# Optimization experiments

Hardware: AMD Instinct MI355X
Metric: run time of the kernel (lower is better)

Reference implementation:

```python
import jax, jax.numpy as jnp
import numpy as np

EPS = 1e-6

def _l2norm(t):
    # F.normalize over channel axis (axis=1) of (B, dk, L)
    n = jnp.sqrt(jnp.sum(t * t, axis=1, keepdims=True))
    return t / jnp.maximum(n, EPS)

def setup_inputs() -> dict:
    key = jax.random.key(0)
    ks = jax.random.split(key, 8)
    B, Cin, Cenc, dk, dv, H, W = 2, 64, 96, 64, 64, 96, 96
    return {
        "x": jax.random.normal(ks[0], (B, Cin, H, W), dtype=jnp.float32),
        "x_enc": jax.random.normal(ks[1], (B, Cenc, H, W), dtype=jnp.float32),
        "Wq": jax.random.normal(ks[2], (dk, Cenc), dtype=jnp.float32) * 0.05,
        "bq": jax.random.normal(ks[3], (dk,), dtype=jnp.float32) * 0.05,
        "Wk": jax.random.normal(ks[4], (dk, Cenc), dtype=jnp.float32) * 0.05,
        "bk": jax.random.normal(ks[5], (dk,), dtype=jnp.float32) * 0.05,
        "Wv": jax.random.normal(ks[6], (dv, Cin), dtype=jnp.float32) * 0.05,
        "bv": jax.random.normal(ks[7], (dv,), dtype=jnp.float32) * 0.05,
    }

def reference(x, x_enc, Wq, bq, Wk, bk, Wv, bv):
    B, _, H, W = x.shape
    L = H * W
    # 1x1 conv projections == channel matmuls, then flatten spatial dims
    Q = (jnp.einsum('bchw,kc->bkhw', x_enc, Wq) + bq[None, :, None, None]).reshape(B, -1, L)
    K = (jnp.einsum('bchw,kc->bkhw', x_enc, Wk) + bk[None, :, None, None]).reshape(B, -1, L)
    V = (jnp.einsum('bchw,kc->bkhw', x, Wv) + bv[None, :, None, None]).reshape(B, -1, L)
    # per-position L2 normalization over the dk channel axis ('l2' mode)
    Q = _l2norm(Q)
    K = _l2norm(K)
    # A[b,i,j] = sum_q Q[b,q,i] * K[b,q,j], softmax over j
    A = jax.nn.softmax(jnp.einsum('bqi,bqj->bij', Q, K), axis=-1)  # (B, L, L)
    R = jnp.einsum('bij,bvj->bvi', A, V)  # (B, dv, L)
    return R.reshape(B, -1, H, W)
```

## Files before the change

### kernel.cpp

```cpp
#include <hip/hip_runtime.h>
#include <hip/hip_bf16.h>
#include <math.h>

#define NB   2
#define CIN  64
#define CENC 96
#define DK   64
#define DV   64
#define LL   9216
#define QBLK 128
#define KVBLK 64
#define NQT  (LL/QBLK)
#define LOG2E 1.44269504088896340736f

typedef __attribute__((ext_vector_type(8))) short short8;
typedef __attribute__((ext_vector_type(4))) float f32x4;
typedef __attribute__((ext_vector_type(2))) unsigned int uint2v;
typedef unsigned int uint;

__device__ inline void gload16(const void* g, void* l) {
    __builtin_amdgcn_global_load_lds(
        (const __attribute__((address_space(1))) unsigned int*)g,
        (__attribute__((address_space(3))) unsigned int*)l, 16, 0, 0);
}

__device__ inline unsigned short f2bf(float f) {
    union { float f; uint u; } v; v.f = f;
    uint r = (v.u + 0x7FFFu + ((v.u >> 16) & 1u)) >> 16;
    return (unsigned short)r;
}

__device__ inline uint pack_bf16x2(float lo, float hi) {
    __hip_bfloat162 h = __float22bfloat162_rn(float2{lo, hi});
    union { __hip_bfloat162 h; uint u; } cvt; cvt.h = h;
    return cvt.u;
}

__global__ __launch_bounds__(256) void proj_qk_kernel(
    const float* __restrict__ x_enc,
    const float* __restrict__ Wq, const float* __restrict__ bq,
    const float* __restrict__ Wk, const float* __restrict__ bk,
    unsigned short* __restrict__ Qb, unsigned short* __restrict__ Kb)
{
    __shared__ float Wt[2][CENC * 64];
    const int tid = threadIdx.x;
    for (int idx = tid; idx < DK * CENC; idx += 256) {
        int k = idx / CENC, c = idx - k * CENC;
        Wt[0][c * 64 + (k ^ (c & 31))] = Wq[idx];
        Wt[1][c * 64 + (k ^ (c & 31))] = Wk[idx];
    }
    __syncthreads();

    const int w    = __builtin_amdgcn_readfirstlane(tid >> 6);
    const int lane = tid & 63;
    const int gw   = blockIdx.x * 4 + w;
    const int p0g  = gw * 16;
    const int b    = p0g / LL;
    const int p0   = p0g - b * LL;

    float qa[16], ka[16];
    const float bqv = bq[lane], bkv = bk[lane];
#pragma unroll
    for (int p = 0; p < 16; ++p) { qa[p] = bqv; ka[p] = bkv; }

    const float* xp = x_enc + (size_t)b * CENC * LL + p0;
#pragma unroll 4
    for (int c = 0; c < CENC; ++c) {
        const float wq = Wt[0][c * 64 + (lane ^ (c & 31))];
        const float wk = Wt[1][c * 64 + (lane ^ (c & 31))];
        const float* xc = xp + (size_t)c * LL;
#pragma unroll
        for (int p = 0; p < 16; ++p) {
            const float xv = xc[p];
            qa[p] = fmaf(wq, xv, qa[p]);
            ka[p] = fmaf(wk, xv, ka[p]);
        }
    }

    unsigned short* qrow = Qb + (size_t)(b * LL + p0) * 64 + lane;
    unsigned short* krow = Kb + (size_t)(b * LL + p0) * 64 + lane;
#pragma unroll
    for (int p = 0; p < 16; ++p) {
        float sq = qa[p] * qa[p];
        float sk = ka[p] * ka[p];
#pragma unroll
        for (int m = 1; m < 64; m <<= 1) {
            sq += __shfl_xor(sq, m, 64);
            sk += __shfl_xor(sk, m, 64);
        }
        qrow[(size_t)p * 64] = f2bf(qa[p] * (1.f / fmaxf(sqrtf(sq), 1e-6f)));
        krow[(size_t)p * 64] = f2bf(ka[p] * (1.f / fmaxf(sqrtf(sk), 1e-6f)));
    }
}

__global__ __launch_bounds__(256) void proj_v_kernel(
    const float* __restrict__ x,
    const float* __restrict__ Wv, const float* __restrict__ bv,
    unsigned short* __restrict__ Vt)
{
    __shared__ float Wt[CIN * 64];
    __shared__ unsigned short Vl[64 * 64];
    const int tid = threadIdx.x;
    for (int idx = tid; idx < DV * CIN; idx += 256) {
        int v = idx / CIN, c = idx - v * CIN;
        Wt[c * 64 + (v ^ (c & 31))] = Wv[idx];
    }
    __syncthreads();

    const int w    = __builtin_amdgcn_readfirstlane(tid >> 6);
    const int lane = tid & 63;
    const int l0g  = blockIdx.x * 64;
    const int b    = l0g / LL;
    const int l0   = l0g - b * LL;
    const int p0   = w * 16;

    float va[16];
    const float bvv = bv[lane];
#pragma unroll
    for (int p = 0; p < 16; ++p) va[p] = bvv;

    const float* xp = x + (size_t)b * CIN * LL + l0 + p0;
#pragma unroll 4
    for (int c = 0; c < CIN; ++c) {
        const float wv = Wt[c * 64 + (lane ^ (c & 31))];
        const float* xc = xp + (size_t)c * LL;
#pragma unroll
        for (int p = 0; p < 16; ++p) va[p] = fmaf(wv, xc[p], va[p]);
    }
#pragma unroll
    for (int p = 0; p < 16; ++p) Vl[(p0 + p) * 64 + lane] = f2bf(va[p]);
    __syncthreads();

    const int v = tid & 63, w2 = tid >> 6;
    uint pk[8];
#pragma unroll
    for (int j = 0; j < 8; ++j)
        pk[j] = (uint)Vl[(w2 * 16 + 2 * j) * 64 + v] |
                ((uint)Vl[(w2 * 16 + 2 * j + 1) * 64 + v] << 16);
    uint4* dst = (uint4*)(Vt + (size_t)b * 64 * LL + (size_t)v * LL + l0 + w2 * 16);
    dst[0] = make_uint4(pk[0], pk[1], pk[2], pk[3]);
    dst[1] = make_uint4(pk[4], pk[5], pk[6], pk[7]);
}

__global__ __launch_bounds__(256, 3) void flash_kernel(
    const unsigned short* __restrict__ Qb,
    const unsigned short* __restrict__ Kb,
    const unsigned short* __restrict__ Vt,
    float* __restrict__ Sp, float* __restrict__ Rp,
    int JS, int nt)
{
    __shared__ unsigned short Kl[2][KVBLK * 64];
    __shared__ unsigned short Vl[2][64 * KVBLK];
    __shared__ unsigned short Pl[4 * 32 * 64];

    const int bid0  = blockIdx.x;
    const int chunk = gridDim.x >> 3;
    const int bid   = (bid0 & 7) * chunk + (bid0 >> 3);

    const int qt  = bid % NQT;
    const int js  = (bid / NQT) % JS;
    const int b   = bid / (NQT * JS);
    const int tid = threadIdx.x;
    const int w = tid >> 6, lane = tid & 63;
    const int li = lane & 15, hi = lane >> 4;
    const int i0 = qt * QBLK + w * 32;

    short8 qf[2][2];
#pragma unroll
    for (int it = 0; it < 2; ++it)
#pragma unroll
        for (int kc = 0; kc < 2; ++kc)
            qf[it][kc] = *(const short8*)(Qb + ((size_t)(b * LL + i0 + it * 16 + li)) * 64 + hi * 8 + kc * 32);

    const int a0 = li * 128 + (( hi     ) ^ (li & 7)) * 16;
    const int a1 = li * 128 + ((hi + 4) ^ (li & 7)) * 16;

    const int o0 = w * 1024 + lane * 16;
    const int o1 = o0 + 4096;
    const int r0 = o0 >> 7, r1 = o1 >> 7;
    const int c0 = ((o0 >> 4) & 7) ^ (r0 & 7);
    const int c1 = ((o1 >> 4) & 7) ^ (r1 & 7);

    const unsigned short* KbB = Kb + (size_t)b * LL * 64;
    const unsigned short* VtB = Vt + (size_t)b * 64 * LL;

    f32x4 racc[2][4];
#pragma unroll
    for (int it = 0; it < 2; ++it)
#pragma unroll
        for (int vt = 0; vt < 4; ++vt)
            racc[it][vt] = (f32x4){0.f, 0.f, 0.f, 0.f};
    float ssum[2] = {0.f, 0.f};

    char* Plw = (char*)Pl + w * 4096;

    int j0 = js * (nt * KVBLK);
    gload16(KbB + (size_t)(j0 + r0) * 64 + c0 * 8, (char*)Kl[0] + w * 1024);
    gload16(KbB + (size_t)(j0 + r1) * 64 + c1 * 8, (char*)Kl[0] + w * 1024 + 4096);
    gload16(VtB + (size_t)r0 * LL + j0 + c0 * 8, (char*)Vl[0] + w * 1024);
    gload16(VtB + (size_t)r1 * LL + j0 + c1 * 8, (char*)Vl[0] + w * 1024 + 4096);

    for (int t = 0; t < nt; ++t, j0 += KVBLK) {
        __syncthreads();
        const int bb = t & 1;
        if (t + 1 < nt) {
            const int j1 = j0 + KVBLK;
            gload16(KbB + (size_t)(j1 + r0) * 64 + c0 * 8, (char*)Kl[bb ^ 1] + w * 1024);
            gload16(KbB + (size_t)(j1 + r1) * 64 + c1 * 8, (char*)Kl[bb ^ 1] + w * 1024 + 4096);
            gload16(VtB + (size_t)r0 * LL + j1 + c0 * 8, (char*)Vl[bb ^ 1] + w * 1024);
            gload16(VtB + (size_t)r1 * LL + j1 + c1 * 8, (char*)Vl[bb ^ 1] + w * 1024 + 4096);
        }
        const char* Klb = (const char*)Kl[bb];
        const char* Vlb = (const char*)Vl[bb];

#pragma unroll
        for (int jt = 0; jt < 4; ++jt) {
            const short8 k0 = *(const short8*)(Klb + jt * 2048 + a0);
            const short8 k1 = *(const short8*)(Klb + jt * 2048 + a1);
#pragma unroll
            for (int it = 0; it < 2; ++it) {
                f32x4 acc = (f32x4){0.f, 0.f, 0.f, 0.f};
                acc = __builtin_amdgcn_mfma_f32_16x16x32_bf16(k0, qf[it][0], acc, 0, 0, 0);
                acc = __builtin_amdgcn_mfma_f32_16x16x32_bf16(k1, qf[it][1], acc, 0, 0, 0);
                float p0 = __builtin_amdgcn_exp2f(fmaf(acc[0], LOG2E, -LOG2E));
                float p1 = __builtin_amdgcn_exp2f(fmaf(acc[1], LOG2E, -LOG2E));
                float p2 = __builtin_amdgcn_exp2f(fmaf(acc[2], LOG2E, -LOG2E));
                float p3 = __builtin_amdgcn_exp2f(fmaf(acc[3], LOG2E, -LOG2E));
                ssum[it] += (p0 + p1) + (p2 + p3);
                uint2v u;
                u.x = pack_bf16x2(p0, p1);
                u.y = pack_bf16x2(p2, p3);
                *(uint2v*)(Plw + (it * 16 + li) * 128
                               + (((jt * 2 + (hi >> 1)) ^ (li & 7)) * 16) + (hi & 1) * 8) = u;
            }
        }
        __asm__ volatile("" ::: "memory");

#pragma unroll
        for (int jc = 0; jc < 2; ++jc) {
            const short8 pa0 = *(const short8*)(Plw + (0 * 16 + li) * 128 + (((jc * 4 + hi) ^ (li & 7)) * 16));
            const short8 pa1 = *(const short8*)(Plw + (1 * 16 + li) * 128 + (((jc * 4 + hi) ^ (li & 7)) * 16));
            const int av = jc ? a1 : a0;
#pragma unroll
            for (int vt = 0; vt < 4; ++vt) {
                const short8 vb = *(const short8*)(Vlb + vt * 2048 + av);
                racc[0][vt] = __builtin_amdgcn_mfma_f32_16x16x32_bf16(pa0, vb, racc[0][vt], 0, 0, 0);
                racc[1][vt] = __builtin_amdgcn_mfma_f32_16x16x32_bf16(pa1, vb, racc[1][vt], 0, 0, 0);
            }
        }
        __asm__ volatile("" ::: "memory");
    }

#pragma unroll
    for (int it = 0; it < 2; ++it) {
        float s = ssum[it];
        s += __shfl_xor(s, 16, 64);
        s += __shfl_xor(s, 32, 64);
        if (hi == 0) Sp[(size_t)(b * JS + js) * LL + i0 + it * 16 + li] = s;
    }
    const size_t rBase = (size_t)(b * JS + js) * 64;
#pragma unroll
    for (int it = 0; it < 2; ++it)
#pragma unroll
        for (int vt = 0; vt < 4; ++vt) {
            float4 val = make_float4(racc[it][vt][0], racc[it][vt][1], racc[it][vt][2], racc[it][vt][3]);
            *(float4*)&Rp[(rBase + vt * 16 + li) * LL + i0 + it * 16 + hi * 4] = val;
        }
}

__global__ __launch_bounds__(256) void combine_kernel(
    const float* __restrict__ Sp, const float* __restrict__ Rp,
    float* __restrict__ out, int JS)
{
    size_t g4 = ((size_t)blockIdx.x * 256 + threadIdx.x) * 4;
    int l = (int)(g4 % LL);
    int v = (int)((g4 / LL) % 64);
    int b = (int)(g4 / ((size_t)64 * LL));
    float4 s = make_float4(0.f, 0.f, 0.f, 0.f);
    float4 r = make_float4(0.f, 0.f, 0.f, 0.f);
    for (int js = 0; js < JS; ++js) {
        const float4 sv = *(const float4*)&Sp[(size_t)(b * JS + js) * LL + l];
        const float4 rv = *(const float4*)&Rp[((size_t)(b * JS + js) * 64 + v) * LL + l];
        s.x += sv.x; s.y += sv.y; s.z += sv.z; s.w += sv.w;
        r.x += rv.x; r.y += rv.y; r.z += rv.z; r.w += rv.w;
    }
    *(float4*)&out[g4] = make_float4(r.x / s.x, r.y / s.y, r.z / s.z, r.w / s.w);
}

extern "C" void kernel_launch(void* const* d_in, const int* in_sizes, int n_in,
                              void* d_out, int out_size, void* d_ws, size_t ws_size,
                              hipStream_t stream) {
    (void)in_sizes; (void)n_in; (void)out_size;
    const float* x     = (const float*)d_in[0];
    const float* x_enc = (const float*)d_in[1];
    const float* Wq    = (const float*)d_in[2];
    const float* bq    = (const float*)d_in[3];
    const float* Wk    = (const float*)d_in[4];
    const float* bk    = (const float*)d_in[5];
    const float* Wv    = (const float*)d_in[6];
    const float* bv    = (const float*)d_in[7];
    float* out = (float*)d_out;
    char* ws = (char*)d_ws;

    const size_t nBF = (size_t)NB * LL * 64 * 2;
    unsigned short* Qb = (unsigned short*)ws;
    unsigned short* Kb = (unsigned short*)(ws + nBF);
    unsigned short* Vt = (unsigned short*)(ws + 2 * nBF);

    int JS = 8;
    while (JS > 1) {
        size_t need = 3 * nBF + (size_t)NB * JS * LL * 4 + (size_t)NB * JS * 64 * LL * 4;
        if (need <= ws_size) break;
        JS >>= 1;
    }
    float* Sp = (float*)(ws + 3 * nBF);
    float* Rp = Sp + (size_t)NB * JS * LL;
    int nt = (LL / JS) / KVBLK;

    proj_qk_kernel<<<NB * LL / 64, 256, 0, stream>>>(x_enc, Wq, bq, Wk, bk, Qb, Kb);
    proj_v_kernel <<<NB * LL / 64, 256, 0, stream>>>(x, Wv, bv, Vt);
    flash_kernel  <<<NB * JS * NQT, 256, 0, stream>>>(Qb, Kb, Vt, Sp, Rp, JS, nt);
    combine_kernel<<<(NB * 64 * LL) / 1024, 256, 0, stream>>>(Sp, Rp, out, JS);
}
```

Before: 117.6 us.

## Switch flash kernel to 32x32 MFMA with register-resident P and fused projection

The attention kernel moves from 16x16x32 to 32x32x16 bf16 MFMA tiles with 64 queries per wave and a 256-query block. The softmax probabilities are repacked in registers with permlane32 swaps instead of going through a shared-memory P buffer. LOG2E is folded into the Q normalization so the exp2 needs no extra FMA, and s_setprio is set around the MFMA groups. The Q/K and V projections are merged into one launch, and the key split rises to 12. The cost is higher register pressure, occupancy capped at 2 blocks per CU, and a larger partial-result buffer for the combine step.

```diff
diff --git a/kernel.cpp b/kernel.cpp
--- a/kernel.cpp
+++ b/kernel.cpp
@@ -8,14 +8,14 @@
 #define DK   64
 #define DV   64
 #define LL   9216
-#define QBLK 128
+#define QBLK 256
 #define KVBLK 64
 #define NQT  (LL/QBLK)
 #define LOG2E 1.44269504088896340736f
 
-typedef __attribute__((ext_vector_type(8))) short short8;
-typedef __attribute__((ext_vector_type(4))) float f32x4;
-typedef __attribute__((ext_vector_type(2))) unsigned int uint2v;
+typedef __attribute__((ext_vector_type(8)))  short short8;
+typedef __attribute__((ext_vector_type(16))) float f32x16;
+typedef __attribute__((ext_vector_type(2)))  unsigned int uint2v;
 typedef unsigned int uint;
 
 __device__ inline void gload16(const void* g, void* l) {
@@ -36,113 +36,127 @@
     return cvt.u;
 }
 
-__global__ __launch_bounds__(256) void proj_qk_kernel(
-    const float* __restrict__ x_enc,
+__device__ inline void plswap(uint& a, uint& b) {
+#if __has_builtin(__builtin_amdgcn_permlane32_swap)
+    uint2v r = __builtin_amdgcn_permlane32_swap(a, b, false, false);
+    a = r.x; b = r.y;
+#else
+    const int lane = threadIdx.x & 63;
+    uint t = (lane < 32) ? b : a;
+    t = __shfl_xor(t, 32, 64);
+    uint an = (lane < 32) ? a : t;
+    uint bn = (lane < 32) ? t : b;
+    a = an; b = bn;
+#endif
+}
+
+__global__ __launch_bounds__(256) void proj_kernel(
+    const float* __restrict__ x, const float* __restrict__ x_enc,
     const float* __restrict__ Wq, const float* __restrict__ bq,
     const float* __restrict__ Wk, const float* __restrict__ bk,
-    unsigned short* __restrict__ Qb, unsigned short* __restrict__ Kb)
+    const float* __restrict__ Wv, const float* __restrict__ bv,
+    unsigned short* __restrict__ Qb, unsigned short* __restrict__ Kb,
+    unsigned short* __restrict__ Vt, int nqk)
 {
-    __shared__ float Wt[2][CENC * 64];
+    __shared__ float sh[2 * CENC * 64];
     const int tid = threadIdx.x;
-    for (int idx = tid; idx < DK * CENC; idx += 256) {
-        int k = idx / CENC, c = idx - k * CENC;
-        Wt[0][c * 64 + (k ^ (c & 31))] = Wq[idx];
-        Wt[1][c * 64 + (k ^ (c & 31))] = Wk[idx];
-    }
-    __syncthreads();
-
-    const int w    = __builtin_amdgcn_readfirstlane(tid >> 6);
-    const int lane = tid & 63;
-    const int gw   = blockIdx.x * 4 + w;
-    const int p0g  = gw * 16;
-    const int b    = p0g / LL;
-    const int p0   = p0g - b * LL;
-
-    float qa[16], ka[16];
-    const float bqv = bq[lane], bkv = bk[lane];
-#pragma unroll
-    for (int p = 0; p < 16; ++p) { qa[p] = bqv; ka[p] = bkv; }
-
-    const float* xp = x_enc + (size_t)b * CENC * LL + p0;
+
+    if ((int)blockIdx.x < nqk) {
+        float* Wt0 = sh;
+        float* Wt1 = sh + CENC * 64;
+        for (int idx = tid; idx < DK * CENC; idx += 256) {
+            int k = idx / CENC, c = idx - k * CENC;
+            Wt0[c * 64 + (k ^ (c & 31))] = Wq[idx];
+            Wt1[c * 64 + (k ^ (c & 31))] = Wk[idx];
+        }
+        __syncthreads();
+
+        const int w    = __builtin_amdgcn_readfirstlane(tid >> 6);
+        const int lane = tid & 63;
+        const int gw   = blockIdx.x * 4 + w;
+        const int p0g  = gw * 16;
+        const int b    = p0g / LL;
+        const int p0   = p0g - b * LL;
+
+        float qa[16], ka[16];
+        const float bqv = bq[lane], bkv = bk[lane];
+#pragma unroll
+        for (int p = 0; p < 16; ++p) { qa[p] = bqv; ka[p] = bkv; }
+
+        const float* xp = x_enc + (size_t)b * CENC * LL + p0;
 #pragma unroll 4
-    for (int c = 0; c < CENC; ++c) {
-        const float wq = Wt[0][c * 64 + (lane ^ (c & 31))];
-        const float wk = Wt[1][c * 64 + (lane ^ (c & 31))];
-        const float* xc = xp + (size_t)c * LL;
+        for (int c = 0; c < CENC; ++c) {
+            const float wq = Wt0[c * 64 + (lane ^ (c & 31))];
+            const float wk = Wt1[c * 64 + (lane ^ (c & 31))];
+            const float* xc = xp + (size_t)c * LL;
+#pragma unroll
+            for (int p = 0; p < 16; ++p) {
+                const float xv = xc[p];
+                qa[p] = fmaf(wq, xv, qa[p]);
+                ka[p] = fmaf(wk, xv, ka[p]);
+            }
+        }
+
+        unsigned short* qrow = Qb + (size_t)(b * LL + p0) * 64 + lane;
+        unsigned short* krow = Kb + (size_t)(b * LL + p0) * 64 + lane;
 #pragma unroll
         for (int p = 0; p < 16; ++p) {
-            const float xv = xc[p];
-            qa[p] = fmaf(wq, xv, qa[p]);
-            ka[p] = fmaf(wk, xv, ka[p]);
-        }
-    }
-
-    unsigned short* qrow = Qb + (size_t)(b * LL + p0) * 64 + lane;
-    unsigned short* krow = Kb + (size_t)(b * LL + p0) * 64 + lane;
-#pragma unroll
-    for (int p = 0; p < 16; ++p) {
-        float sq = qa[p] * qa[p];
-        float sk = ka[p] * ka[p];
-#pragma unroll
-        for (int m = 1; m < 64; m <<= 1) {
-            sq += __shfl_xor(sq, m, 64);
-            sk += __shfl_xor(sk, m, 64);
-        }
-        qrow[(size_t)p * 64] = f2bf(qa[p] * (1.f / fmaxf(sqrtf(sq), 1e-6f)));
-        krow[(size_t)p * 64] = f2bf(ka[p] * (1.f / fmaxf(sqrtf(sk), 1e-6f)));
-    }
-}
-
-__global__ __launch_bounds__(256) void proj_v_kernel(
-    const float* __restrict__ x,
-    const float* __restrict__ Wv, const float* __restrict__ bv,
-    unsigned short* __restrict__ Vt)
-{
-    __shared__ float Wt[CIN * 64];
-    __shared__ unsigned short Vl[64 * 64];
-    const int tid = threadIdx.x;
-    for (int idx = tid; idx < DV * CIN; idx += 256) {
-        int v = idx / CIN, c = idx - v * CIN;
-        Wt[c * 64 + (v ^ (c & 31))] = Wv[idx];
-    }
-    __syncthreads();
-
-    const int w    = __builtin_amdgcn_readfirstlane(tid >> 6);
-    const int lane = tid & 63;
-    const int l0g  = blockIdx.x * 64;
-    const int b    = l0g / LL;
-    const int l0   = l0g - b * LL;
-    const int p0   = w * 16;
-
-    float va[16];
-    const float bvv = bv[lane];
-#pragma unroll
-    for (int p = 0; p < 16; ++p) va[p] = bvv;
-
-    const float* xp = x + (size_t)b * CIN * LL + l0 + p0;
+            float sq = qa[p] * qa[p];
+            float sk = ka[p] * ka[p];
+#pragma unroll
+            for (int m = 1; m < 64; m <<= 1) {
+                sq += __shfl_xor(sq, m, 64);
+                sk += __shfl_xor(sk, m, 64);
+            }
+            qrow[(size_t)p * 64] = f2bf(qa[p] * (LOG2E / fmaxf(sqrtf(sq), 1e-6f)));
+            krow[(size_t)p * 64] = f2bf(ka[p] * (1.f / fmaxf(sqrtf(sk), 1e-6f)));
+        }
+    } else {
+        float* Wt = sh;
+        unsigned short* Vsh = (unsigned short*)(sh + CIN * 64);
+        for (int idx = tid; idx < DV * CIN; idx += 256) {
+            int v = idx / CIN, c = idx - v * CIN;
+            Wt[c * 64 + (v ^ (c & 31))] = Wv[idx];
+        }
+        __syncthreads();
+
+        const int w    = __builtin_amdgcn_readfirstlane(tid >> 6);
+        const int lane = tid & 63;
+        const int l0g  = ((int)blockIdx.x - nqk) * 64;
+        const int b    = l0g / LL;
+        const int l0   = l0g - b * LL;
+        const int p0   = w * 16;
+
+        float va[16];
+        const float bvv = bv[lane];
+#pragma unroll
+        for (int p = 0; p < 16; ++p) va[p] = bvv;
+
+        const float* xp = x + (size_t)b * CIN * LL + l0 + p0;
 #pragma unroll 4
-    for (int c = 0; c < CIN; ++c) {
-        const float wv = Wt[c * 64 + (lane ^ (c & 31))];
-        const float* xc = xp + (size_t)c * LL;
-#pragma unroll
-        for (int p = 0; p < 16; ++p) va[p] = fmaf(wv, xc[p], va[p]);
-    }
-#pragma unroll
-    for (int p = 0; p < 16; ++p) Vl[(p0 + p) * 64 + lane] = f2bf(va[p]);
-    __syncthreads();
-
-    const int v = tid & 63, w2 = tid >> 6;
-    uint pk[8];
-#pragma unroll
-    for (int j = 0; j < 8; ++j)
-        pk[j] = (uint)Vl[(w2 * 16 + 2 * j) * 64 + v] |
-                ((uint)Vl[(w2 * 16 + 2 * j + 1) * 64 + v] << 16);
-    uint4* dst = (uint4*)(Vt + (size_t)b * 64 * LL + (size_t)v * LL + l0 + w2 * 16);
-    dst[0] = make_uint4(pk[0], pk[1], pk[2], pk[3]);
-    dst[1] = make_uint4(pk[4], pk[5], pk[6], pk[7]);
-}
-
-__global__ __launch_bounds__(256, 3) void flash_kernel(
+        for (int c = 0; c < CIN; ++c) {
+            const float wv = Wt[c * 64 + (lane ^ (c & 31))];
+            const float* xc = xp + (size_t)c * LL;
+#pragma unroll
+            for (int p = 0; p < 16; ++p) va[p] = fmaf(wv, xc[p], va[p]);
+        }
+#pragma unroll
+        for (int p = 0; p < 16; ++p) Vsh[(p0 + p) * 64 + lane] = f2bf(va[p]);
+        __syncthreads();
+
+        const int v = tid & 63, w2 = tid >> 6;
+        uint pk[8];
+#pragma unroll
+        for (int j = 0; j < 8; ++j)
+            pk[j] = (uint)Vsh[(w2 * 16 + 2 * j) * 64 + v] |
+                    ((uint)Vsh[(w2 * 16 + 2 * j + 1) * 64 + v] << 16);
+        uint4* dst = (uint4*)(Vt + (size_t)b * 64 * LL + (size_t)v * LL + l0 + w2 * 16);
+        dst[0] = make_uint4(pk[0], pk[1], pk[2], pk[3]);
+        dst[1] = make_uint4(pk[4], pk[5], pk[6], pk[7]);
+    }
+}
+
+__global__ __launch_bounds__(256, 2) void flash_kernel(
     const unsigned short* __restrict__ Qb,
     const unsigned short* __restrict__ Kb,
     const unsigned short* __restrict__ Vt,
@@ -151,7 +165,6 @@
 {
     __shared__ unsigned short Kl[2][KVBLK * 64];
     __shared__ unsigned short Vl[2][64 * KVBLK];
-    __shared__ unsigned short Pl[4 * 32 * 64];
 
     const int bid0  = blockIdx.x;
     const int chunk = gridDim.x >> 3;
@@ -162,18 +175,15 @@
     const int b   = bid / (NQT * JS);
     const int tid = threadIdx.x;
     const int w = tid >> 6, lane = tid & 63;
-    const int li = lane & 15, hi = lane >> 4;
-    const int i0 = qt * QBLK + w * 32;
-
-    short8 qf[2][2];
-#pragma unroll
-    for (int it = 0; it < 2; ++it)
-#pragma unroll
-        for (int kc = 0; kc < 2; ++kc)
-            qf[it][kc] = *(const short8*)(Qb + ((size_t)(b * LL + i0 + it * 16 + li)) * 64 + hi * 8 + kc * 32);
-
-    const int a0 = li * 128 + (( hi     ) ^ (li & 7)) * 16;
-    const int a1 = li * 128 + ((hi + 4) ^ (li & 7)) * 16;
+    const int ln = lane & 31, h = lane >> 5;
+    const int i0w = qt * QBLK + w * 64;
+
+    short8 qf[2][4];
+#pragma unroll
+    for (int ig = 0; ig < 2; ++ig)
+#pragma unroll
+        for (int kc = 0; kc < 4; ++kc)
+            qf[ig][kc] = *(const short8*)(Qb + ((size_t)(b * LL + i0w + ig * 32 + ln)) * 64 + kc * 16 + h * 8);
 
     const int o0 = w * 1024 + lane * 16;
     const int o1 = o0 + 4096;
@@ -184,17 +194,16 @@
     const unsigned short* KbB = Kb + (size_t)b * LL * 64;
     const unsigned short* VtB = Vt + (size_t)b * 64 * LL;
 
-    f32x4 racc[2][4];
-#pragma unroll
-    for (int it = 0; it < 2; ++it)
-#pragma unroll
-        for (int vt = 0; vt < 4; ++vt)
-            racc[it][vt] = (f32x4){0.f, 0.f, 0.f, 0.f};
+    f32x16 racc[2][2];
+#pragma unroll
+    for (int ig = 0; ig < 2; ++ig)
+#pragma unroll
+        for (int vg = 0; vg < 2; ++vg)
+#pragma unroll
+            for (int r = 0; r < 16; ++r) racc[ig][vg][r] = 0.f;
     float ssum[2] = {0.f, 0.f};
 
-    char* Plw = (char*)Pl + w * 4096;
-
-    int j0 = js * (nt * KVBLK);
+    int j0 = js * nt * KVBLK;
     gload16(KbB + (size_t)(j0 + r0) * 64 + c0 * 8, (char*)Kl[0] + w * 1024);
     gload16(KbB + (size_t)(j0 + r1) * 64 + c1 * 8, (char*)Kl[0] + w * 1024 + 4096);
     gload16(VtB + (size_t)r0 * LL + j0 + c0 * 8, (char*)Vl[0] + w * 1024);
@@ -214,57 +223,84 @@
         const char* Vlb = (const char*)Vl[bb];
 
 #pragma unroll
-        for (int jt = 0; jt < 4; ++jt) {
-            const short8 k0 = *(const short8*)(Klb + jt * 2048 + a0);
-            const short8 k1 = *(const short8*)(Klb + jt * 2048 + a1);
-#pragma unroll
-            for (int it = 0; it < 2; ++it) {
-                f32x4 acc = (f32x4){0.f, 0.f, 0.f, 0.f};
-                acc = __builtin_amdgcn_mfma_f32_16x16x32_bf16(k0, qf[it][0], acc, 0, 0, 0);
-                acc = __builtin_amdgcn_mfma_f32_16x16x32_bf16(k1, qf[it][1], acc, 0, 0, 0);
-                float p0 = __builtin_amdgcn_exp2f(fmaf(acc[0], LOG2E, -LOG2E));
-                float p1 = __builtin_amdgcn_exp2f(fmaf(acc[1], LOG2E, -LOG2E));
-                float p2 = __builtin_amdgcn_exp2f(fmaf(acc[2], LOG2E, -LOG2E));
-                float p3 = __builtin_amdgcn_exp2f(fmaf(acc[3], LOG2E, -LOG2E));
-                ssum[it] += (p0 + p1) + (p2 + p3);
-                uint2v u;
-                u.x = pack_bf16x2(p0, p1);
-                u.y = pack_bf16x2(p2, p3);
-                *(uint2v*)(Plw + (it * 16 + li) * 128
-                               + (((jt * 2 + (hi >> 1)) ^ (li & 7)) * 16) + (hi & 1) * 8) = u;
-            }
-        }
-        __asm__ volatile("" ::: "memory");
-
-#pragma unroll
-        for (int jc = 0; jc < 2; ++jc) {
-            const short8 pa0 = *(const short8*)(Plw + (0 * 16 + li) * 128 + (((jc * 4 + hi) ^ (li & 7)) * 16));
-            const short8 pa1 = *(const short8*)(Plw + (1 * 16 + li) * 128 + (((jc * 4 + hi) ^ (li & 7)) * 16));
-            const int av = jc ? a1 : a0;
-#pragma unroll
-            for (int vt = 0; vt < 4; ++vt) {
-                const short8 vb = *(const short8*)(Vlb + vt * 2048 + av);
-                racc[0][vt] = __builtin_amdgcn_mfma_f32_16x16x32_bf16(pa0, vb, racc[0][vt], 0, 0, 0);
-                racc[1][vt] = __builtin_amdgcn_mfma_f32_16x16x32_bf16(pa1, vb, racc[1][vt], 0, 0, 0);
-            }
-        }
-        __asm__ volatile("" ::: "memory");
-    }
-
-#pragma unroll
-    for (int it = 0; it < 2; ++it) {
-        float s = ssum[it];
-        s += __shfl_xor(s, 16, 64);
-        s += __shfl_xor(s, 32, 64);
-        if (hi == 0) Sp[(size_t)(b * JS + js) * LL + i0 + it * 16 + li] = s;
+        for (int jt = 0; jt < 2; ++jt) {
+            f32x16 sacc[2];
+#pragma unroll
+            for (int ig = 0; ig < 2; ++ig)
+#pragma unroll
+                for (int r = 0; r < 16; ++r) sacc[ig][r] = 0.f;
+
+            __builtin_amdgcn_s_setprio(1);
+#pragma unroll
+            for (int kc = 0; kc < 4; ++kc) {
+                const int rowK = jt * 32 + ln;
+                const short8 kf = *(const short8*)(Klb + rowK * 128 + (((kc << 1) + h) ^ (rowK & 7)) * 16);
+                sacc[0] = __builtin_amdgcn_mfma_f32_32x32x16_bf16(kf, qf[0][kc], sacc[0], 0, 0, 0);
+                sacc[1] = __builtin_amdgcn_mfma_f32_32x32x16_bf16(kf, qf[1][kc], sacc[1], 0, 0, 0);
+            }
+            __builtin_amdgcn_s_setprio(0);
+
+            short8 pf[2][2];
+#pragma unroll
+            for (int ig = 0; ig < 2; ++ig) {
+                float p[16];
+#pragma unroll
+                for (int r = 0; r < 16; ++r) p[r] = __builtin_amdgcn_exp2f(sacc[ig][r]);
+                float s0 = 0.f;
+#pragma unroll
+                for (int r = 0; r < 16; r += 4) s0 += (p[r] + p[r + 1]) + (p[r + 2] + p[r + 3]);
+                ssum[ig] += s0;
+                uint u0[4], u1[4];
+#pragma unroll
+                for (int g = 0; g < 4; ++g) {
+                    u0[g] = pack_bf16x2(p[4 * g], p[4 * g + 1]);
+                    u1[g] = pack_bf16x2(p[4 * g + 2], p[4 * g + 3]);
+                }
+#pragma unroll
+                for (int c = 0; c < 2; ++c) {
+                    uint a0 = u0[2 * c], b0 = u0[2 * c + 1];
+                    uint a1 = u1[2 * c], b1 = u1[2 * c + 1];
+                    plswap(a0, b0);
+                    plswap(a1, b1);
+                    union { uint u[4]; short8 s; } P;
+                    P.u[0] = a0; P.u[1] = a1; P.u[2] = b0; P.u[3] = b1;
+                    pf[ig][c] = P.s;
+                }
+            }
+
+            __builtin_amdgcn_s_setprio(1);
+#pragma unroll
+            for (int c = 0; c < 2; ++c) {
+                const int kcv = 2 * jt + c;
+#pragma unroll
+                for (int vg = 0; vg < 2; ++vg) {
+                    const int rowV = vg * 32 + ln;
+                    const short8 vf = *(const short8*)(Vlb + rowV * 128 + (((kcv << 1) + h) ^ (rowV & 7)) * 16);
+                    racc[0][vg] = __builtin_amdgcn_mfma_f32_32x32x16_bf16(pf[0][c], vf, racc[0][vg], 0, 0, 0);
+                    racc[1][vg] = __builtin_amdgcn_mfma_f32_32x32x16_bf16(pf[1][c], vf, racc[1][vg], 0, 0, 0);
+                }
+            }
+            __builtin_amdgcn_s_setprio(0);
+        }
+    }
+
+#pragma unroll
+    for (int ig = 0; ig < 2; ++ig) {
+        float s = ssum[ig] + __shfl_xor(ssum[ig], 32, 64);
+        if (h == 0) Sp[(size_t)(b * JS + js) * LL + i0w + ig * 32 + ln] = s;
     }
     const size_t rBase = (size_t)(b * JS + js) * 64;
 #pragma unroll
-    for (int it = 0; it < 2; ++it)
-#pragma unroll
-        for (int vt = 0; vt < 4; ++vt) {
-            float4 val = make_float4(racc[it][vt][0], racc[it][vt][1], racc[it][vt][2], racc[it][vt][3]);
-            *(float4*)&Rp[(rBase + vt * 16 + li) * LL + i0 + it * 16 + hi * 4] = val;
+    for (int ig = 0; ig < 2; ++ig)
+#pragma unroll
+        for (int vg = 0; vg < 2; ++vg) {
+            float* dst = Rp + (rBase + vg * 32 + ln) * (size_t)LL + i0w + ig * 32 + 4 * h;
+#pragma unroll
+            for (int rr = 0; rr < 4; ++rr) {
+                float4 val = make_float4(racc[ig][vg][4 * rr + 0], racc[ig][vg][4 * rr + 1],
+                                         racc[ig][vg][4 * rr + 2], racc[ig][vg][4 * rr + 3]);
+                *(float4*)&dst[8 * rr] = val;
+            }
         }
 }
 
@@ -307,18 +343,21 @@
     unsigned short* Kb = (unsigned short*)(ws + nBF);
     unsigned short* Vt = (unsigned short*)(ws + 2 * nBF);
 
-    int JS = 8;
-    while (JS > 1) {
-        size_t need = 3 * nBF + (size_t)NB * JS * LL * 4 + (size_t)NB * JS * 64 * LL * 4;
-        if (need <= ws_size) break;
-        JS >>= 1;
+    int JS = 12;
+    {
+        const int cand[3] = {12, 8, 4};
+        for (int ci = 0; ci < 3; ++ci) {
+            JS = cand[ci];
+            size_t need = 3 * nBF + (size_t)NB * JS * LL * 4 + (size_t)NB * JS * 64 * LL * 4;
+            if (need <= ws_size) break;
+        }
     }
     float* Sp = (float*)(ws + 3 * nBF);
     float* Rp = Sp + (size_t)NB * JS * LL;
     int nt = (LL / JS) / KVBLK;
 
-    proj_qk_kernel<<<NB * LL / 64, 256, 0, stream>>>(x_enc, Wq, bq, Wk, bk, Qb, Kb);
-    proj_v_kernel <<<NB * LL / 64, 256, 0, stream>>>(x, Wv, bv, Vt);
-    flash_kernel  <<<NB * JS * NQT, 256, 0, stream>>>(Qb, Kb, Vt, Sp, Rp, JS, nt);
+    const int nqk = NB * LL / 64;
+    proj_kernel  <<<2 * nqk, 256, 0, stream>>>(x, x_enc, Wq, bq, Wk, bk, Wv, bv, Qb, Kb, Vt, nqk);
+    flash_kernel <<<NB * JS * NQT, 256, 0, stream>>>(Qb, Kb, Vt, Sp, Rp, JS, nt);
     combine_kernel<<<(NB * 64 * LL) / 1024, 256, 0, stream>>>(Sp, Rp, out, JS);
 }
```

Result: faster. 109.0 us (-7.3%).
